# Kernel tuning notes

Measured on AMD Instinct MI355X. Metric: run time of the kernel, lower is better.

Reference implementation:

```python
import jax, jax.numpy as jnp
import numpy as np

EPS = 1e-12  # matches torch F.normalize default eps
TEMP = 0.1


def _gram(x):
    # L2-normalize rows; for unit vectors 1 - 0.5*||xi-xj||^2 == xi . xj
    n = x / jnp.maximum(jnp.linalg.norm(x, axis=-1, keepdims=True), EPS)
    return n @ n.T  # [N, N]


def setup_inputs() -> dict:
    key = jax.random.key(0)
    k1, k2, k3, k4 = jax.random.split(key, 4)
    N, D = 4096, 512
    return {
        "fm_rgb": jax.random.normal(k1, (N, D), dtype=jnp.float32),
        "fm_depth": jax.random.normal(k2, (N, D), dtype=jnp.float32),
        "fm_ir": jax.random.normal(k3, (N, D), dtype=jnp.float32),
        "fm_t": jax.random.normal(k4, (N, D), dtype=jnp.float32),
    }


def reference(fm_rgb, fm_depth, fm_ir, fm_t):
    G_rgb = _gram(fm_rgb)
    G_depth = _gram(fm_depth)
    G_ir = _gram(fm_ir)
    G_t = _gram(fm_t)
    inv_t = 1.0 / TEMP
    loss_rgb = jnp.mean((G_t * inv_t - G_rgb * inv_t) ** 2)
    loss_depth = jnp.mean((G_t * inv_t - G_depth * inv_t) ** 2)
    loss_ir = jnp.mean((G_t * inv_t - G_ir * inv_t) ** 2)
    return loss_rgb + loss_depth + loss_ir
```

## Files before the change

kernel.cpp:

```cpp
#include <hip/hip_runtime.h>
#include <hip/hip_bf16.h>


typedef __attribute__((ext_vector_type(8))) short short8;
typedef __attribute__((ext_vector_type(8))) unsigned short ushort8;
typedef __attribute__((ext_vector_type(4))) float floatx4;

#define N_ROWS 4096
#define DDIM   512
#define NT_BYTES     ((size_t)4 * DDIM * N_ROWS * 2)
#define RSC_BYTES    ((size_t)4 * N_ROWS * 4)
#define SLICE_FLOATS ((size_t)112 * 16384)
#define NSPLIT 4
#define LOSS_SCALE 5.9604644775390625e-06f

__device__ __forceinline__ const float* sel_mod(int mod, const float* a,
                                                const float* b, const float* c,
                                                const float* d) {
  return mod == 0 ? a : mod == 1 ? b : mod == 2 ? c : d;
}

__global__ __launch_bounds__(256) void rownorm_kernel(
    const float* __restrict__ in0, const float* __restrict__ in1,
    const float* __restrict__ in2, const float* __restrict__ in3,
    float* __restrict__ rscale) {
  int t = threadIdx.x;
  int w = t >> 6, lane = t & 63;
  int base = blockIdx.x * 8;
#pragma unroll
  for (int i = 0; i < 2; ++i) {
    int g = base + w * 2 + i;
    int mod = g >> 12, r = g & 4095;
    const float* X = sel_mod(mod, in0, in1, in2, in3);
    const float4* rp = (const float4*)(X + (size_t)r * DDIM);
    float4 a = rp[lane];
    float4 b = rp[lane + 64];
    float ss = a.x * a.x + a.y * a.y + a.z * a.z + a.w * a.w +
               b.x * b.x + b.y * b.y + b.z * b.z + b.w * b.w;
#pragma unroll
    for (int off = 32; off > 0; off >>= 1) ss += __shfl_down(ss, off, 64);
    if (lane == 0) rscale[g] = 1.0f / fmaxf(sqrtf(ss), 1e-12f);
  }
}

__global__ __launch_bounds__(256) void transpose_kernel(
    const float* __restrict__ in0, const float* __restrict__ in1,
    const float* __restrict__ in2, const float* __restrict__ in3,
    const float* __restrict__ rscale, unsigned short* __restrict__ nT) {
  int mod = blockIdx.z;
  int k0 = blockIdx.x * 64;
  int c0 = blockIdx.y * 128;
  const float* X = sel_mod(mod, in0, in1, in2, in3);

  __shared__ float lrsc[64];
  __shared__ unsigned short tile[128][72];

  int t = threadIdx.x;
  if (t < 64) lrsc[t] = rscale[mod * N_ROWS + k0 + t];
  __syncthreads();

#pragma unroll
  for (int it = 0; it < 8; ++it) {
    int idx = it * 256 + t;
    int r = idx >> 5;
    int c4 = idx & 31;
    float4 v = ((const float4*)(X + (size_t)(k0 + r) * DDIM + c0))[c4];
    float sc = lrsc[r];
    __hip_bfloat16 h0 = __float2bfloat16(v.x * sc);
    __hip_bfloat16 h1 = __float2bfloat16(v.y * sc);
    __hip_bfloat16 h2 = __float2bfloat16(v.z * sc);
    __hip_bfloat16 h3 = __float2bfloat16(v.w * sc);
    tile[c4 * 4 + 0][r] = *(unsigned short*)&h0;
    tile[c4 * 4 + 1][r] = *(unsigned short*)&h1;
    tile[c4 * 4 + 2][r] = *(unsigned short*)&h2;
    tile[c4 * 4 + 3][r] = *(unsigned short*)&h3;
  }
  __syncthreads();

#pragma unroll
  for (int it = 0; it < 4; ++it) {
    int idx = it * 256 + t;
    int c = idx >> 3;
    int g = idx & 7;
    ushort8 v = *(const ushort8*)&tile[c][g * 8];
    *(ushort8*)(nT + ((size_t)mod * DDIM + c0 + c) * N_ROWS + k0 + g * 8) = v;
  }
}

__device__ __forceinline__ void stage_tiles(
    const unsigned short* __restrict__ Abase,
    const unsigned short* __restrict__ Bbase, int k0,
    unsigned short* lsA, unsigned short* lsB, int wave, int lane) {
  int srow = lane >> 3;
  int scol = ((lane & 7) ^ srow) * 8;
#pragma unroll
  for (int c = 0; c < 4; ++c) {
    int base_row = wave * 32 + c * 8;
    const unsigned short* ga =
        Abase + (size_t)(base_row + srow) * N_ROWS + k0 + scol;
    const unsigned short* gb =
        Bbase + (size_t)(base_row + srow) * N_ROWS + k0 + scol;
    __builtin_amdgcn_global_load_lds(
        (__attribute__((address_space(1))) void*)(void*)ga,
        (__attribute__((address_space(3))) void*)(void*)&lsA[base_row * 64],
        16, 0, 0);
    __builtin_amdgcn_global_load_lds(
        (__attribute__((address_space(1))) void*)(void*)gb,
        (__attribute__((address_space(3))) void*)(void*)&lsB[base_row * 64],
        16, 0, 0);
  }
}

__device__ __forceinline__ void compute_tiles(
    const unsigned short* lsA, const unsigned short* lsB,
    floatx4 acc[4][4], int wr, int wc, int lm, int lq) {
#pragma unroll
  for (int ks = 0; ks < 2; ++ks) {
    int slot = (ks * 4 + lq) ^ (lm & 7);
    short8 af[4], bf[4];
#pragma unroll
    for (int mi = 0; mi < 4; ++mi) {
      int row = wr + mi * 16 + lm;
      af[mi] = *(const short8*)&lsA[row * 64 + slot * 8];
    }
#pragma unroll
    for (int ni = 0; ni < 4; ++ni) {
      int row = wc + ni * 16 + lm;
      bf[ni] = *(const short8*)&lsB[row * 64 + slot * 8];
    }
#pragma unroll
    for (int mi = 0; mi < 4; ++mi)
#pragma unroll
      for (int ni = 0; ni < 4; ++ni)
        acc[mi][ni] = __builtin_amdgcn_mfma_f32_16x16x32_bf16(
            af[mi], bf[ni], acc[mi][ni], 0, 0, 0);
  }
}

__global__ __launch_bounds__(256) void gram_frob_kernel(
    const unsigned short* __restrict__ nT, float* __restrict__ Cbuf) {
  __shared__ unsigned short ls[2][2][128 * 64];

  const int pa[7] = {3, 0, 1, 2, 3, 3, 3};
  const int pb[7] = {3, 0, 1, 2, 0, 1, 2};

  int tile = blockIdx.x;
  int prod = blockIdx.y;
  int kbase = blockIdx.z * 1024;
  int a0 = (tile >> 2) * 128;
  int b0 = (tile & 3) * 128;
  const unsigned short* Abase = nT + ((size_t)pa[prod] * DDIM + a0) * N_ROWS;
  const unsigned short* Bbase = nT + ((size_t)pb[prod] * DDIM + b0) * N_ROWS;

  int t = threadIdx.x;
  int wave = t >> 6;
  int lane = t & 63;
  int wr = (wave >> 1) * 64;
  int wc = (wave & 1) * 64;
  int lm = lane & 15;
  int lq = lane >> 4;

  floatx4 zero = {0.f, 0.f, 0.f, 0.f};
  floatx4 acc[4][4];
#pragma unroll
  for (int mi = 0; mi < 4; ++mi)
#pragma unroll
    for (int ni = 0; ni < 4; ++ni) acc[mi][ni] = zero;

  stage_tiles(Abase, Bbase, kbase, ls[0][0], ls[0][1], wave, lane);
  __syncthreads();
  int k0 = kbase + 64;
  for (int i = 0; i < 7; ++i) {
    stage_tiles(Abase, Bbase, k0, ls[1][0], ls[1][1], wave, lane);
    compute_tiles(ls[0][0], ls[0][1], acc, wr, wc, lm, lq);
    __syncthreads();
    stage_tiles(Abase, Bbase, k0 + 64, ls[0][0], ls[0][1], wave, lane);
    compute_tiles(ls[1][0], ls[1][1], acc, wr, wc, lm, lq);
    __syncthreads();
    k0 += 128;
  }
  stage_tiles(Abase, Bbase, kbase + 960, ls[1][0], ls[1][1], wave, lane);
  compute_tiles(ls[0][0], ls[0][1], acc, wr, wc, lm, lq);
  __syncthreads();
  compute_tiles(ls[1][0], ls[1][1], acc, wr, wc, lm, lq);

  float* Cp = Cbuf + (size_t)blockIdx.z * SLICE_FLOATS +
              (size_t)(prod * 16 + tile) * 16384;
#pragma unroll
  for (int mi = 0; mi < 4; ++mi)
#pragma unroll
    for (int ni = 0; ni < 4; ++ni) {
      int j = mi * 4 + ni;
      *(floatx4*)(Cp + (size_t)(j * 256 + t) * 4) = acc[mi][ni];
    }
}

__global__ __launch_bounds__(256) void reduce_kernel(
    const float4* __restrict__ Cbuf, float* __restrict__ out) {
  const float w[7] = {3.f, 1.f, 1.f, 1.f, -2.f, -2.f, -2.f};
  const size_t S4 = SLICE_FLOATS / 4;
  int t = threadIdx.x;
  float s = 0.f;
  size_t stride = (size_t)gridDim.x * 256;
  for (size_t i = (size_t)blockIdx.x * 256 + t; i < S4; i += stride) {
    float4 a = Cbuf[i];
    float4 b = Cbuf[i + S4];
    float4 c = Cbuf[i + 2 * S4];
    float4 d = Cbuf[i + 3 * S4];
    float vx = a.x + b.x + c.x + d.x;
    float vy = a.y + b.y + c.y + d.y;
    float vz = a.z + b.z + c.z + d.z;
    float vw = a.w + b.w + c.w + d.w;
    float ww = w[i >> 16];
    s += ww * (vx * vx + vy * vy + vz * vz + vw * vw);
  }
#pragma unroll
  for (int off = 32; off > 0; off >>= 1) s += __shfl_down(s, off, 64);
  __shared__ float red[4];
  if ((t & 63) == 0) red[t >> 6] = s;
  __syncthreads();
  if (t == 0)
    atomicAdd(out, LOSS_SCALE * (red[0] + red[1] + red[2] + red[3]));
}

extern "C" void kernel_launch(void* const* d_in, const int* in_sizes, int n_in,
                              void* d_out, int out_size, void* d_ws, size_t ws_size,
                              hipStream_t stream) {
  const float* in_rgb   = (const float*)d_in[0];
  const float* in_depth = (const float*)d_in[1];
  const float* in_ir    = (const float*)d_in[2];
  const float* in_t     = (const float*)d_in[3];

  unsigned short* nT = (unsigned short*)d_ws;
  float* rscale = (float*)((char*)d_ws + NT_BYTES);
  float* Cbuf   = (float*)((char*)d_ws + NT_BYTES + RSC_BYTES);

  hipMemsetAsync(d_out, 0, out_size * sizeof(float), stream);

  rownorm_kernel<<<2048, 256, 0, stream>>>(in_rgb, in_depth, in_ir, in_t,
                                           rscale);
  transpose_kernel<<<dim3(64, 4, 4), 256, 0, stream>>>(in_rgb, in_depth, in_ir,
                                                       in_t, rscale, nT);
  gram_frob_kernel<<<dim3(16, 7, NSPLIT), 256, 0, stream>>>(nT, Cbuf);
  reduce_kernel<<<448, 256, 0, stream>>>((const float4*)Cbuf, (float*)d_out);
}
```

Baseline: 120.5 us.

## Switch Gram GEMM to FP8 MFMA and fuse row-norm with transpose

Normalized inputs are now scaled by 16, quantized to FP8 and stored transposed, so the Gram/Frobenius GEMM runs on fp8 MFMA with half the staged bytes and a new XOR swizzle for 128-byte rows. The row-norm and transpose kernels are merged into one preprocess kernel, which saves a launch and a pass over the inputs. The loss scale is adjusted for the 16x pre-scaling. FP8 quantization lowers the accuracy of the loss, and the preprocess grid is smaller, which may underuse the GPU.

```diff
diff --git a/kernel.cpp b/kernel.cpp
--- a/kernel.cpp
+++ b/kernel.cpp
@@ -2,17 +2,15 @@
 #include <hip/hip_bf16.h>
 
 
-typedef __attribute__((ext_vector_type(8))) short short8;
+typedef __attribute__((ext_vector_type(4))) float floatx4;
 typedef __attribute__((ext_vector_type(8))) unsigned short ushort8;
-typedef __attribute__((ext_vector_type(4))) float floatx4;
 
 #define N_ROWS 4096
 #define DDIM   512
-#define NT_BYTES     ((size_t)4 * DDIM * N_ROWS * 2)
-#define RSC_BYTES    ((size_t)4 * N_ROWS * 4)
+#define NT8_BYTES    ((size_t)4 * DDIM * N_ROWS)
 #define SLICE_FLOATS ((size_t)112 * 16384)
 #define NSPLIT 4
-#define LOSS_SCALE 5.9604644775390625e-06f
+#define LOSS_SCALE 9.094947017729282e-11f
 
 __device__ __forceinline__ const float* sel_mod(int mod, const float* a,
                                                 const float* b, const float* c,
@@ -20,18 +18,23 @@
   return mod == 0 ? a : mod == 1 ? b : mod == 2 ? c : d;
 }
 
-__global__ __launch_bounds__(256) void rownorm_kernel(
+__global__ __launch_bounds__(256) void preprocess_kernel(
     const float* __restrict__ in0, const float* __restrict__ in1,
     const float* __restrict__ in2, const float* __restrict__ in3,
-    float* __restrict__ rscale) {
+    unsigned char* __restrict__ nT8) {
+  int mod = blockIdx.y;
+  int k0 = blockIdx.x * 64;
+  const float* X = sel_mod(mod, in0, in1, in2, in3) + (size_t)k0 * DDIM;
+
+  __shared__ float rsc[64];
+  __shared__ unsigned short tile[128][72];
+
   int t = threadIdx.x;
   int w = t >> 6, lane = t & 63;
-  int base = blockIdx.x * 8;
-#pragma unroll
-  for (int i = 0; i < 2; ++i) {
-    int g = base + w * 2 + i;
-    int mod = g >> 12, r = g & 4095;
-    const float* X = sel_mod(mod, in0, in1, in2, in3);
+
+#pragma unroll
+  for (int i = 0; i < 16; ++i) {
+    int r = w * 16 + i;
     const float4* rp = (const float4*)(X + (size_t)r * DDIM);
     float4 a = rp[lane];
     float4 b = rp[lane + 64];
@@ -39,107 +42,113 @@
                b.x * b.x + b.y * b.y + b.z * b.z + b.w * b.w;
 #pragma unroll
     for (int off = 32; off > 0; off >>= 1) ss += __shfl_down(ss, off, 64);
-    if (lane == 0) rscale[g] = 1.0f / fmaxf(sqrtf(ss), 1e-12f);
-  }
-}
-
-__global__ __launch_bounds__(256) void transpose_kernel(
-    const float* __restrict__ in0, const float* __restrict__ in1,
-    const float* __restrict__ in2, const float* __restrict__ in3,
-    const float* __restrict__ rscale, unsigned short* __restrict__ nT) {
-  int mod = blockIdx.z;
-  int k0 = blockIdx.x * 64;
-  int c0 = blockIdx.y * 128;
-  const float* X = sel_mod(mod, in0, in1, in2, in3);
-
-  __shared__ float lrsc[64];
-  __shared__ unsigned short tile[128][72];
-
-  int t = threadIdx.x;
-  if (t < 64) lrsc[t] = rscale[mod * N_ROWS + k0 + t];
-  __syncthreads();
-
-#pragma unroll
-  for (int it = 0; it < 8; ++it) {
-    int idx = it * 256 + t;
-    int r = idx >> 5;
-    int c4 = idx & 31;
-    float4 v = ((const float4*)(X + (size_t)(k0 + r) * DDIM + c0))[c4];
-    float sc = lrsc[r];
-    __hip_bfloat16 h0 = __float2bfloat16(v.x * sc);
-    __hip_bfloat16 h1 = __float2bfloat16(v.y * sc);
-    __hip_bfloat16 h2 = __float2bfloat16(v.z * sc);
-    __hip_bfloat16 h3 = __float2bfloat16(v.w * sc);
-    tile[c4 * 4 + 0][r] = *(unsigned short*)&h0;
-    tile[c4 * 4 + 1][r] = *(unsigned short*)&h1;
-    tile[c4 * 4 + 2][r] = *(unsigned short*)&h2;
-    tile[c4 * 4 + 3][r] = *(unsigned short*)&h3;
-  }
-  __syncthreads();
-
-#pragma unroll
-  for (int it = 0; it < 4; ++it) {
-    int idx = it * 256 + t;
-    int c = idx >> 3;
-    int g = idx & 7;
-    ushort8 v = *(const ushort8*)&tile[c][g * 8];
-    *(ushort8*)(nT + ((size_t)mod * DDIM + c0 + c) * N_ROWS + k0 + g * 8) = v;
+    if (lane == 0) rsc[r] = 16.0f / fmaxf(sqrtf(ss), 1e-12f);
+  }
+  __syncthreads();
+
+  for (int p = 0; p < 4; ++p) {
+#pragma unroll
+    for (int it = 0; it < 8; ++it) {
+      int idx = it * 256 + t;
+      int r = idx >> 5;
+      int c4 = idx & 31;
+      float4 v = ((const float4*)(X + (size_t)r * DDIM + p * 128))[c4];
+      float sc = rsc[r];
+      __hip_bfloat16 h0 = __float2bfloat16(v.x * sc);
+      __hip_bfloat16 h1 = __float2bfloat16(v.y * sc);
+      __hip_bfloat16 h2 = __float2bfloat16(v.z * sc);
+      __hip_bfloat16 h3 = __float2bfloat16(v.w * sc);
+      tile[c4 * 4 + 0][r] = *(unsigned short*)&h0;
+      tile[c4 * 4 + 1][r] = *(unsigned short*)&h1;
+      tile[c4 * 4 + 2][r] = *(unsigned short*)&h2;
+      tile[c4 * 4 + 3][r] = *(unsigned short*)&h3;
+    }
+    __syncthreads();
+#pragma unroll
+    for (int it = 0; it < 2; ++it) {
+      int idx = it * 256 + t;
+      int c = idx >> 2;
+      int g = idx & 3;
+      ushort8 u0 = *(const ushort8*)&tile[c][g * 16];
+      ushort8 u1 = *(const ushort8*)&tile[c][g * 16 + 8];
+      float f[16];
+#pragma unroll
+      for (int j = 0; j < 8; ++j) {
+        f[j] = __uint_as_float(((unsigned int)(unsigned short)u0[j]) << 16);
+        f[8 + j] = __uint_as_float(((unsigned int)(unsigned short)u1[j]) << 16);
+      }
+      unsigned int wds[4];
+#pragma unroll
+      for (int q = 0; q < 4; ++q) {
+        unsigned int pk = __builtin_amdgcn_cvt_pk_fp8_f32(f[4 * q], f[4 * q + 1], 0, 0);
+        pk = __builtin_amdgcn_cvt_pk_fp8_f32(f[4 * q + 2], f[4 * q + 3], pk, 1);
+        wds[q] = pk;
+      }
+      uint4 out = {wds[0], wds[1], wds[2], wds[3]};
+      *(uint4*)(nT8 + ((size_t)(mod * DDIM + p * 128 + c)) * N_ROWS + k0 +
+                g * 16) = out;
+    }
+    __syncthreads();
   }
 }
 
 __device__ __forceinline__ void stage_tiles(
-    const unsigned short* __restrict__ Abase,
-    const unsigned short* __restrict__ Bbase, int k0,
-    unsigned short* lsA, unsigned short* lsB, int wave, int lane) {
-  int srow = lane >> 3;
-  int scol = ((lane & 7) ^ srow) * 8;
+    const unsigned char* __restrict__ Abase,
+    const unsigned char* __restrict__ Bbase, int k0,
+    unsigned char* lsA, unsigned char* lsB, int wave, int lane) {
+  int rr = lane >> 3;
+  int s = lane & 7;
 #pragma unroll
   for (int c = 0; c < 4; ++c) {
-    int base_row = wave * 32 + c * 8;
-    const unsigned short* ga =
-        Abase + (size_t)(base_row + srow) * N_ROWS + k0 + scol;
-    const unsigned short* gb =
-        Bbase + (size_t)(base_row + srow) * N_ROWS + k0 + scol;
+    int base = wave * 32 + c * 8;
+    int row = base + rr;
+    int gc = s ^ ((row >> 1) & 7);
+    const unsigned char* ga = Abase + (size_t)row * N_ROWS + k0 + gc * 16;
+    const unsigned char* gb = Bbase + (size_t)row * N_ROWS + k0 + gc * 16;
     __builtin_amdgcn_global_load_lds(
         (__attribute__((address_space(1))) void*)(void*)ga,
-        (__attribute__((address_space(3))) void*)(void*)&lsA[base_row * 64],
+        (__attribute__((address_space(3))) void*)(void*)&lsA[base * 128],
         16, 0, 0);
     __builtin_amdgcn_global_load_lds(
         (__attribute__((address_space(1))) void*)(void*)gb,
-        (__attribute__((address_space(3))) void*)(void*)&lsB[base_row * 64],
+        (__attribute__((address_space(3))) void*)(void*)&lsB[base * 128],
         16, 0, 0);
   }
 }
 
 __device__ __forceinline__ void compute_tiles(
-    const unsigned short* lsA, const unsigned short* lsB,
+    const unsigned char* lsA, const unsigned char* lsB,
     floatx4 acc[4][4], int wr, int wc, int lm, int lq) {
 #pragma unroll
-  for (int ks = 0; ks < 2; ++ks) {
-    int slot = (ks * 4 + lq) ^ (lm & 7);
-    short8 af[4], bf[4];
+  for (int ks = 0; ks < 4; ++ks) {
+    int j = ks * 4 + lq;
+    int cg = j >> 1;
+    int sub = (j & 1) * 8;
+    long long af[4], bf[4];
 #pragma unroll
     for (int mi = 0; mi < 4; ++mi) {
       int row = wr + mi * 16 + lm;
-      af[mi] = *(const short8*)&lsA[row * 64 + slot * 8];
+      int slot = cg ^ ((row >> 1) & 7);
+      af[mi] = *(const long long*)&lsA[row * 128 + slot * 16 + sub];
     }
 #pragma unroll
     for (int ni = 0; ni < 4; ++ni) {
       int row = wc + ni * 16 + lm;
-      bf[ni] = *(const short8*)&lsB[row * 64 + slot * 8];
+      int slot = cg ^ ((row >> 1) & 7);
+      bf[ni] = *(const long long*)&lsB[row * 128 + slot * 16 + sub];
     }
 #pragma unroll
     for (int mi = 0; mi < 4; ++mi)
 #pragma unroll
       for (int ni = 0; ni < 4; ++ni)
-        acc[mi][ni] = __builtin_amdgcn_mfma_f32_16x16x32_bf16(
+        acc[mi][ni] = __builtin_amdgcn_mfma_f32_16x16x32_fp8_fp8(
             af[mi], bf[ni], acc[mi][ni], 0, 0, 0);
   }
 }
 
 __global__ __launch_bounds__(256) void gram_frob_kernel(
-    const unsigned short* __restrict__ nT, float* __restrict__ Cbuf) {
-  __shared__ unsigned short ls[2][2][128 * 64];
+    const unsigned char* __restrict__ nT8, float* __restrict__ Cbuf) {
+  __shared__ unsigned char ls[2][2][128 * 128];
 
   const int pa[7] = {3, 0, 1, 2, 3, 3, 3};
   const int pb[7] = {3, 0, 1, 2, 0, 1, 2};
@@ -149,8 +158,8 @@
   int kbase = blockIdx.z * 1024;
   int a0 = (tile >> 2) * 128;
   int b0 = (tile & 3) * 128;
-  const unsigned short* Abase = nT + ((size_t)pa[prod] * DDIM + a0) * N_ROWS;
-  const unsigned short* Bbase = nT + ((size_t)pb[prod] * DDIM + b0) * N_ROWS;
+  const unsigned char* Abase = nT8 + ((size_t)pa[prod] * DDIM + a0) * N_ROWS;
+  const unsigned char* Bbase = nT8 + ((size_t)pb[prod] * DDIM + b0) * N_ROWS;
 
   int t = threadIdx.x;
   int wave = t >> 6;
@@ -169,17 +178,17 @@
 
   stage_tiles(Abase, Bbase, kbase, ls[0][0], ls[0][1], wave, lane);
   __syncthreads();
-  int k0 = kbase + 64;
-  for (int i = 0; i < 7; ++i) {
+  int k0 = kbase + 128;
+  for (int i = 0; i < 3; ++i) {
     stage_tiles(Abase, Bbase, k0, ls[1][0], ls[1][1], wave, lane);
     compute_tiles(ls[0][0], ls[0][1], acc, wr, wc, lm, lq);
     __syncthreads();
-    stage_tiles(Abase, Bbase, k0 + 64, ls[0][0], ls[0][1], wave, lane);
+    stage_tiles(Abase, Bbase, k0 + 128, ls[0][0], ls[0][1], wave, lane);
     compute_tiles(ls[1][0], ls[1][1], acc, wr, wc, lm, lq);
     __syncthreads();
-    k0 += 128;
-  }
-  stage_tiles(Abase, Bbase, kbase + 960, ls[1][0], ls[1][1], wave, lane);
+    k0 += 256;
+  }
+  stage_tiles(Abase, Bbase, kbase + 896, ls[1][0], ls[1][1], wave, lane);
   compute_tiles(ls[0][0], ls[0][1], acc, wr, wc, lm, lq);
   __syncthreads();
   compute_tiles(ls[1][0], ls[1][1], acc, wr, wc, lm, lq);
@@ -231,16 +240,13 @@
   const float* in_ir    = (const float*)d_in[2];
   const float* in_t     = (const float*)d_in[3];
 
-  unsigned short* nT = (unsigned short*)d_ws;
-  float* rscale = (float*)((char*)d_ws + NT_BYTES);
-  float* Cbuf   = (float*)((char*)d_ws + NT_BYTES + RSC_BYTES);
+  unsigned char* nT8 = (unsigned char*)d_ws;
+  float* Cbuf = (float*)((char*)d_ws + NT8_BYTES);
 
   hipMemsetAsync(d_out, 0, out_size * sizeof(float), stream);
 
-  rownorm_kernel<<<2048, 256, 0, stream>>>(in_rgb, in_depth, in_ir, in_t,
-                                           rscale);
-  transpose_kernel<<<dim3(64, 4, 4), 256, 0, stream>>>(in_rgb, in_depth, in_ir,
-                                                       in_t, rscale, nT);
-  gram_frob_kernel<<<dim3(16, 7, NSPLIT), 256, 0, stream>>>(nT, Cbuf);
+  preprocess_kernel<<<dim3(64, 4), 256, 0, stream>>>(in_rgb, in_depth, in_ir,
+                                                     in_t, nT8);
+  gram_frob_kernel<<<dim3(16, 7, NSPLIT), 256, 0, stream>>>(nT8, Cbuf);
   reduce_kernel<<<448, 256, 0, stream>>>((const float4*)Cbuf, (float*)d_out);
 }
```

After: 120.3 us. Within noise of the previous version (-0.2%).
